# Optimization experiments

Measured on AMD Instinct MI355X. Metric: run time of the kernel, lower is better.

Reference implementation:

```python
import jax, jax.numpy as jnp
import numpy as np

WS = 7
NH = 4

def _rel_idx(ws):
    ch, cw = np.meshgrid(np.arange(ws), np.arange(ws), indexing='ij')
    cf = np.stack([ch.ravel(), cw.ravel()])  # [2, ws*ws]
    rel = cf[:, :, None] - cf[:, None, :]
    rel = rel.transpose(1, 2, 0)
    rel[:, :, 0] += ws - 1
    rel[:, :, 1] += ws - 1
    rel[:, :, 0] *= 2 * ws - 1
    return jnp.asarray(rel.sum(-1), dtype=jnp.int32)  # [N, N]

def layernorm(x, g, b, eps=1e-5):
    m = jnp.mean(x, -1, keepdims=True)
    v = jnp.var(x, -1, keepdims=True)
    return (x - m) * jax.lax.rsqrt(v + eps) * g + b

def setup_inputs() -> dict:
    key = jax.random.key(0)
    ks = jax.random.split(key, 8)
    B, HH, WW, C = 32, 56, 56, 128
    hid = 512
    s = 0.02
    return {
        'x': jax.random.normal(ks[0], (B, HH * WW, C), jnp.float32),
        'H': HH, 'W': WW,
        'norm1_g': jnp.ones((C,), jnp.float32),
        'norm1_b': jnp.zeros((C,), jnp.float32),
        'qkv_w': jax.random.normal(ks[1], (3 * C, C), jnp.float32) * s,
        'qkv_b': jnp.zeros((3 * C,), jnp.float32),
        'rel_bias_table': jax.random.normal(ks[2], ((2 * WS - 1) ** 2, NH), jnp.float32) * s,
        'rel_idx': _rel_idx(WS),
        'proj_w': jax.random.normal(ks[3], (C, C), jnp.float32) * s,
        'proj_b': jnp.zeros((C,), jnp.float32),
        'norm2_g': jnp.ones((C,), jnp.float32),
        'norm2_b': jnp.zeros((C,), jnp.float32),
        'mlp_w1': jax.random.normal(ks[4], (hid, C), jnp.float32) * s,
        'mlp_b1': jnp.zeros((hid,), jnp.float32),
        'mlp_w2': jax.random.normal(ks[5], (C, hid), jnp.float32) * s,
        'mlp_b2': jnp.zeros((C,), jnp.float32),
    }

def swin_block(x, H, W, norm1_g, norm1_b, qkv_w, qkv_b, rel_bias_table, rel_idx,
               proj_w, proj_b, norm2_g, norm2_b, mlp_w1, mlp_b1, mlp_w2, mlp_b2,
               shift=3, ws=WS, nh=NH):
    B, L, C = x.shape
    N = ws * ws
    hd = C // nh
    scale = hd ** -0.5
    shortcut = x
    h = layernorm(x, norm1_g, norm1_b).reshape(B, H, W, C)
    if shift > 0:
        h = jnp.roll(h, (-shift, -shift), axis=(1, 2))
    # window partition -> [B*nW, N, C]
    h = h.reshape(B, H // ws, ws, W // ws, ws, C).transpose(0, 1, 3, 2, 4, 5).reshape(-1, N, C)
    # attention (no mask in source forward)
    qkv = h @ qkv_w.T + qkv_b  # [B_, N, 3C]
    qkv = qkv.reshape(-1, N, 3, nh, hd).transpose(2, 0, 3, 1, 4)
    q, k, v = qkv[0] * scale, qkv[1], qkv[2]  # [B_, nh, N, hd]
    attn = jnp.einsum('bhnd,bhmd->bhnm', q, k)
    bias = rel_bias_table[rel_idx.reshape(-1)].reshape(N, N, nh).transpose(2, 0, 1)
    attn = jax.nn.softmax(attn + bias[None], axis=-1)
    o = jnp.einsum('bhnm,bhmd->bhnd', attn, v).transpose(0, 2, 1, 3).reshape(-1, N, C)
    o = o @ proj_w.T + proj_b
    # window reverse -> [B, H, W, C]
    o = o.reshape(B, H // ws, W // ws, ws, ws, C).transpose(0, 1, 3, 2, 4, 5).reshape(B, H, W, C)
    if shift > 0:
        o = jnp.roll(o, (shift, shift), axis=(1, 2))
    x = shortcut + o.reshape(B, L, C)
    h2 = layernorm(x, norm2_g, norm2_b)
    h2 = jax.nn.gelu(h2 @ mlp_w1.T + mlp_b1, approximate=False) @ mlp_w2.T + mlp_b2
    return x + h2

def reference(x, H, W, norm1_g, norm1_b, qkv_w, qkv_b, rel_bias_table, rel_idx,
              proj_w, proj_b, norm2_g, norm2_b, mlp_w1, mlp_b1, mlp_w2, mlp_b2):
    return swin_block(x, H, W, norm1_g, norm1_b, qkv_w, qkv_b, rel_bias_table, rel_idx,
                      proj_w, proj_b, norm2_g, norm2_b, mlp_w1, mlp_b1, mlp_w2, mlp_b2)
```

## Files before the change

kernel.cpp:

```cpp
#include <hip/hip_runtime.h>
#include <hip/hip_bf16.h>


#define NWIN 2048

typedef short short8  __attribute__((ext_vector_type(8)));
typedef short short4v __attribute__((ext_vector_type(4)));
typedef float f32x4   __attribute__((ext_vector_type(4)));

union Frag { int i[4]; unsigned u[4]; short8 s; };

#define QKVW_OFF  0
#define PROJW_OFF 49152
#define W1_OFF    65536
#define W2_OFF    131072
#define BIAS_BYTE_OFF 393216

__device__ __forceinline__ short f2bs(float v) {
  __hip_bfloat16 h = __float2bfloat16(v);
  union { __hip_bfloat16 h; short s; } u; u.h = h; return u.s;
}
__device__ __forceinline__ float gelu_f(float v) {
  float u = v * (0.7978845608028654f + 0.03567740814f * v * v);
  return v * __builtin_amdgcn_rcpf(1.f + __expf(-2.f * u));
}

__global__ __launch_bounds__(256) void conv_kernel(
    const float* __restrict__ qkvw, const float* __restrict__ projw,
    const float* __restrict__ w1,   const float* __restrict__ w2,
    const float* __restrict__ tab,  const int* __restrict__ ridx,
    __hip_bfloat16* __restrict__ wsb, float* __restrict__ biasT)
{
  int idx = blockIdx.x * 256 + threadIdx.x;
  if (idx < 49152)       wsb[QKVW_OFF + idx]          = __float2bfloat16(qkvw[idx]);
  else if (idx < 65536)  wsb[PROJW_OFF + idx - 49152] = __float2bfloat16(projw[idx - 49152]);
  else if (idx < 131072) wsb[W1_OFF + idx - 65536]    = __float2bfloat16(w1[idx - 65536]);
  else if (idx < 196608) wsb[W2_OFF + idx - 131072]   = __float2bfloat16(w2[idx - 131072]);
  else if (idx < 212992) {
    int i = idx - 196608;
    int h = i >> 12, m = (i >> 6) & 63, n = i & 63;
    biasT[i] = (m < 49 && n < 49) ? tab[ridx[n*49 + m]*4 + h] : 0.f;
  }
}

__global__ __launch_bounds__(512, 4) void fused_kernel(
    const float* __restrict__ x,
    const float* __restrict__ n1g, const float* __restrict__ n1b,
    const __hip_bfloat16* __restrict__ qkvwb, const float* __restrict__ qkvb,
    const float* __restrict__ biasT,
    const __hip_bfloat16* __restrict__ projwb, const float* __restrict__ projb,
    const float* __restrict__ n2g, const float* __restrict__ n2b,
    const __hip_bfloat16* __restrict__ w1b, const float* __restrict__ b1,
    const __hip_bfloat16* __restrict__ w2b, const float* __restrict__ b2,
    float* __restrict__ out)
{
  __shared__ alignas(16) __hip_bfloat16 hbuf[64][136];
  __shared__ alignas(16) char shmem[34816];
  __hip_bfloat16* const Kl  = (__hip_bfloat16*)shmem;
  __hip_bfloat16* const vTl = (__hip_bfloat16*)(shmem + 17408);
  float*          const x2s = (float*)shmem;
  __hip_bfloat16* const hbA = (__hip_bfloat16*)shmem;
  __hip_bfloat16* const hbB = (__hip_bfloat16*)(shmem + 17408);

  const int tid = threadIdx.x, wave = tid >> 6, lane = tid & 63;
  const int l15 = lane & 15, quad = lane >> 4;
  const int h = wave >> 1, half = wave & 1;
  const int b = blockIdx.x >> 6, wi = (blockIdx.x >> 3) & 7, wj = blockIdx.x & 7;

  {
    float g0 = n1g[lane], g1 = n1g[lane+64], e0 = n1b[lane], e1 = n1b[lane+64];
    float va[7], vb[7];
    #pragma unroll
    for (int i = 0; i < 7; ++i) {
      int n = wave + i*8;
      va[i] = 0.f; vb[i] = 0.f;
      if (n < 49) {
        int r = n / 7, c = n - r * 7;
        int si = wi*7 + r + 3; if (si >= 56) si -= 56;
        int sj = wj*7 + c + 3; if (sj >= 56) sj -= 56;
        const float* xr = x + (b*3136 + si*56 + sj) * 128;
        va[i] = xr[lane]; vb[i] = xr[lane + 64];
      }
    }
    #pragma unroll
    for (int i = 0; i < 7; ++i) {
      int n = wave + i*8;
      if (n < 49) {
        float s = va[i] + vb[i], sq = va[i]*va[i] + vb[i]*vb[i];
        #pragma unroll
        for (int off = 32; off > 0; off >>= 1) {
          s  += __shfl_xor(s,  off);
          sq += __shfl_xor(sq, off);
        }
        float mean = s * 0.0078125f;
        float var  = sq * 0.0078125f - mean*mean;
        float rstd = rsqrtf(var + 1e-5f);
        hbuf[n][lane]    = __float2bfloat16((va[i]-mean)*rstd*g0 + e0);
        hbuf[n][lane+64] = __float2bfloat16((vb[i]-mean)*rstd*g1 + e1);
      }
    }
  }
  __syncthreads();

  {
    f32x4 kacc[4] = {}, vacc[4] = {};
    #pragma unroll
    for (int ks = 0; ks < 4; ++ks) {
      short8 hf[4];
      #pragma unroll
      for (int mt = 0; mt < 4; ++mt)
        hf[mt] = *(const short8*)(&hbuf[mt*16 + l15][ks*32 + quad*8]);
      short8 wfk = *(const short8*)(qkvwb + (128 + wave*16 + l15)*128 + ks*32 + quad*8);
      short8 wfv = *(const short8*)(qkvwb + (256 + wave*16 + l15)*128 + ks*32 + quad*8);
      #pragma unroll
      for (int mt = 0; mt < 4; ++mt) {
        kacc[mt] = __builtin_amdgcn_mfma_f32_16x16x32_bf16(wfk, hf[mt], kacc[mt], 0, 0, 0);
        vacc[mt] = __builtin_amdgcn_mfma_f32_16x16x32_bf16(hf[mt], wfv, vacc[mt], 0, 0, 0);
      }
    }
    {
      const int fo = wave*16 + quad*4;
      float bb[4];
      #pragma unroll
      for (int r = 0; r < 4; ++r) bb[r] = qkvb[128 + fo + r];
      #pragma unroll
      for (int mt = 0; mt < 4; ++mt) {
        int m = mt*16 + l15;
        if (m < 49) {
          short4v pkv;
          #pragma unroll
          for (int r = 0; r < 4; ++r) pkv[r] = f2bs(kacc[mt][r] + bb[r]);
          *(short4v*)(Kl + m*136 + fo) = pkv;
        }
      }
    }
    {
      const int fv = wave*16 + l15;
      const int hh = wave >> 1, d = fv & 31;
      const float bia = qkvb[256 + fv];
      #pragma unroll
      for (int mt = 0; mt < 4; ++mt) {
        int m0 = mt*16 + quad*4;
        #pragma unroll
        for (int r = 0; r < 4; ++r) {
          int m = m0 + r;
          float v = (m < 49) ? (vacc[mt][r] + bia) : 0.f;
          vTl[(hh*32 + d)*64 + ((((m>>3) ^ (d & 7))) << 3) + (m & 7)] = __float2bfloat16(v);
        }
      }
    }
  }

  Frag qfr[2];
  {
    f32x4 qacc[2][2] = {};
    #pragma unroll
    for (int ks = 0; ks < 4; ++ks) {
      short8 hfq[2];
      #pragma unroll
      for (int nt = 0; nt < 2; ++nt)
        hfq[nt] = *(const short8*)(&hbuf[(half*2 + nt)*16 + l15][ks*32 + quad*8]);
      #pragma unroll
      for (int tq = 0; tq < 2; ++tq) {
        short8 wf = *(const short8*)(qkvwb + ((h*2 + tq)*16 + l15)*128 + ks*32 + quad*8);
        #pragma unroll
        for (int nt = 0; nt < 2; ++nt)
          qacc[tq][nt] = __builtin_amdgcn_mfma_f32_16x16x32_bf16(wf, hfq[nt], qacc[tq][nt], 0, 0, 0);
      }
    }
    const float qs = 0.17677669529663687f;
    unsigned pkq[2][2][2];
    #pragma unroll
    for (int tq = 0; tq < 2; ++tq) {
      float bb[4];
      #pragma unroll
      for (int r = 0; r < 4; ++r) bb[r] = qkvb[h*32 + tq*16 + quad*4 + r];
      #pragma unroll
      for (int nt = 0; nt < 2; ++nt)
        #pragma unroll
        for (int i = 0; i < 2; ++i) {
          unsigned lo = (unsigned short)f2bs((qacc[tq][nt][2*i]   + bb[2*i])   * qs);
          unsigned hi = (unsigned short)f2bs((qacc[tq][nt][2*i+1] + bb[2*i+1]) * qs);
          pkq[tq][nt][i] = lo | (hi << 16);
        }
    }
    #pragma unroll
    for (int nt = 0; nt < 2; ++nt)
      #pragma unroll
      for (int p = 0; p < 4; ++p) {
        int sl = (((quad & 1)*2 + (p >> 1)) << 4) | l15;
        int a  = __shfl((int)pkq[0][nt][p & 1], sl);
        int c2 = __shfl((int)pkq[1][nt][p & 1], sl);
        qfr[nt].i[p] = (quad >= 2) ? c2 : a;
      }
  }
  __syncthreads();

  {
    short8 kf[4];
    #pragma unroll
    for (int mt = 0; mt < 4; ++mt)
      kf[mt] = *(const short8*)(Kl + (mt*16 + l15)*136 + h*32 + quad*8);

    f32x4 sacc[4][2] = {};
    #pragma unroll
    for (int mt = 0; mt < 4; ++mt)
      #pragma unroll
      for (int nc = 0; nc < 2; ++nc)
        sacc[mt][nc] = __builtin_amdgcn_mfma_f32_16x16x32_bf16(kf[mt], qfr[nc].s, sacc[mt][nc], 0, 0, 0);

    const float* bT = biasT + h*4096;
    #pragma unroll
    for (int mt = 0; mt < 4; ++mt)
      #pragma unroll
      for (int nc = 0; nc < 2; ++nc)
        #pragma unroll
        for (int r = 0; r < 4; ++r)
          sacc[mt][nc][r] += bT[(mt*16 + quad*4 + r)*64 + (half*2 + nc)*16 + l15];

    unsigned pk[4][2][2];
    #pragma unroll
    for (int nc = 0; nc < 2; ++nc) {
      float mx = -1e30f;
      #pragma unroll
      for (int mt = 0; mt < 3; ++mt)
        #pragma unroll
        for (int r = 0; r < 4; ++r) mx = fmaxf(mx, sacc[mt][nc][r]);
      mx = fmaxf(mx, (quad == 0) ? sacc[3][nc][0] : -1e30f);
      mx = fmaxf(mx, __shfl_xor(mx, 16));
      mx = fmaxf(mx, __shfl_xor(mx, 32));
      float sum = 0.f;
      #pragma unroll
      for (int mt = 0; mt < 3; ++mt)
        #pragma unroll
        for (int r = 0; r < 4; ++r) {
          float e = __expf(sacc[mt][nc][r] - mx);
          sacc[mt][nc][r] = e; sum += e;
        }
      {
        float e = (quad == 0) ? __expf(sacc[3][nc][0] - mx) : 0.f;
        sacc[3][nc][0] = e; sacc[3][nc][1] = 0.f; sacc[3][nc][2] = 0.f; sacc[3][nc][3] = 0.f;
        sum += e;
      }
      sum += __shfl_xor(sum, 16);
      sum += __shfl_xor(sum, 32);
      float inv = 1.f / sum;
      #pragma unroll
      for (int mt = 0; mt < 4; ++mt)
        #pragma unroll
        for (int i = 0; i < 2; ++i) {
          unsigned lo = (unsigned short)f2bs(sacc[mt][nc][2*i]   * inv);
          unsigned hi = (unsigned short)f2bs(sacc[mt][nc][2*i+1] * inv);
          pk[mt][nc][i] = lo | (hi << 16);
        }
    }
    Frag pfr[2][2];
    #pragma unroll
    for (int kt = 0; kt < 2; ++kt)
      #pragma unroll
      for (int nc = 0; nc < 2; ++nc)
        #pragma unroll
        for (int p = 0; p < 4; ++p) {
          int sl = (((quad & 1)*2 + (p >> 1)) << 4) | l15;
          int a  = __shfl((int)pk[kt*2    ][nc][p & 1], sl);
          int c2 = __shfl((int)pk[kt*2 + 1][nc][p & 1], sl);
          pfr[kt][nc].i[p] = (quad >= 2) ? c2 : a;
        }

    f32x4 oacc[2][2] = {};
    #pragma unroll
    for (int kt = 0; kt < 2; ++kt) {
      short8 vf[2];
      #pragma unroll
      for (int dt = 0; dt < 2; ++dt)
        vf[dt] = *(const short8*)(vTl + (h*32 + dt*16 + l15)*64 + (((kt*4 + quad) ^ (l15 & 7)) << 3));
      #pragma unroll
      for (int dt = 0; dt < 2; ++dt)
        #pragma unroll
        for (int nc = 0; nc < 2; ++nc)
          oacc[dt][nc] = __builtin_amdgcn_mfma_f32_16x16x32_bf16(vf[dt], pfr[kt][nc].s, oacc[dt][nc], 0, 0, 0);
    }
    #pragma unroll
    for (int dt = 0; dt < 2; ++dt)
      #pragma unroll
      for (int nc = 0; nc < 2; ++nc) {
        int n = (half*2 + nc)*16 + l15;
        if (n < 49) {
          short4v pkv;
          #pragma unroll
          for (int r = 0; r < 4; ++r) pkv[r] = f2bs(oacc[dt][nc][r]);
          *(short4v*)(&hbuf[n][h*32 + dt*16 + quad*4]) = pkv;
        }
      }
  }
  __syncthreads();

  f32x4 x2v[4];
  {
    const int n = wave * 16 + l15;
    float xres[4][4];
    #pragma unroll
    for (int mt = 0; mt < 4; ++mt) {
      #pragma unroll
      for (int r = 0; r < 4; ++r) {
        int m = mt*16 + quad*4 + r;
        float v = 0.f;
        if (m < 49) {
          int rr = m / 7, cc = m - rr * 7;
          int si = wi*7 + rr + 3; if (si >= 56) si -= 56;
          int sj = wj*7 + cc + 3; if (sj >= 56) sj -= 56;
          v = x[(b*3136 + si*56 + sj) * 128 + n];
        }
        xres[mt][r] = v;
      }
    }
    f32x4 acc[4] = {};
    #pragma unroll
    for (int ks = 0; ks < 4; ++ks) {
      short8 af[4];
      #pragma unroll
      for (int mt = 0; mt < 4; ++mt)
        af[mt] = *(const short8*)(&hbuf[mt*16 + l15][ks*32 + quad*8]);
      short8 bfr = *(const short8*)(projwb + n*128 + ks*32 + quad*8);
      #pragma unroll
      for (int mt = 0; mt < 4; ++mt)
        acc[mt] = __builtin_amdgcn_mfma_f32_16x16x32_bf16(af[mt], bfr, acc[mt], 0, 0, 0);
    }
    float pbv = projb[n];
    #pragma unroll
    for (int mt = 0; mt < 4; ++mt) {
      #pragma unroll
      for (int r = 0; r < 4; ++r) {
        int m = mt*16 + quad*4 + r;
        float v = 0.f;
        if (m < 49) v = acc[mt][r] + pbv + xres[mt][r];
        x2v[mt][r] = v;
        x2s[m*132 + n] = v;
      }
    }
  }
  __syncthreads();

  {
    float g0 = n2g[lane], g1 = n2g[lane+64], e0 = n2b[lane], e1 = n2b[lane+64];
    for (int n = wave; n < 49; n += 8) {
      float v0 = x2s[n*132 + lane], v1 = x2s[n*132 + lane + 64];
      float s = v0 + v1, sq = v0*v0 + v1*v1;
      #pragma unroll
      for (int off = 32; off > 0; off >>= 1) {
        s  += __shfl_xor(s,  off);
        sq += __shfl_xor(sq, off);
      }
      float mean = s * 0.0078125f;
      float var  = sq * 0.0078125f - mean*mean;
      float rstd = rsqrtf(var + 1e-5f);
      hbuf[n][lane]    = __float2bfloat16((v0-mean)*rstd*g0 + e0);
      hbuf[n][lane+64] = __float2bfloat16((v1-mean)*rstd*g1 + e1);
    }
    __hip_bfloat16 z = __float2bfloat16(0.f);
    for (int n = 49 + wave; n < 64; n += 8) {
      hbuf[n][lane] = z; hbuf[n][lane+64] = z;
    }
  }
  __syncthreads();

  f32x4 acc2[4] = {};
  const int fb2 = wave * 16;

  auto G1 = [&](int c, __hip_bfloat16* dst) {
    const int jg = c*128 + wave*16;
    f32x4 a1[4] = {};
    #pragma unroll
    for (int ks = 0; ks < 4; ++ks) {
      short8 lf[4];
      #pragma unroll
      for (int mt = 0; mt < 4; ++mt)
        lf[mt] = *(const short8*)(&hbuf[mt*16 + l15][ks*32 + quad*8]);
      short8 wf = *(const short8*)(w1b + (jg + l15)*128 + ks*32 + quad*8);
      #pragma unroll
      for (int mt = 0; mt < 4; ++mt)
        a1[mt] = __builtin_amdgcn_mfma_f32_16x16x32_bf16(wf, lf[mt], a1[mt], 0, 0, 0);
    }
    float bb[4];
    #pragma unroll
    for (int r = 0; r < 4; ++r) bb[r] = b1[jg + quad*4 + r];
    #pragma unroll
    for (int mt = 0; mt < 4; ++mt) {
      int m = mt*16 + l15;
      short4v pkv;
      #pragma unroll
      for (int r = 0; r < 4; ++r) pkv[r] = f2bs(gelu_f(a1[mt][r] + bb[r]));
      *(short4v*)(dst + m*136 + wave*16 + quad*4) = pkv;
    }
  };
  auto G2 = [&](int c, const __hip_bfloat16* src) {
    #pragma unroll
    for (int ks = 0; ks < 4; ++ks) {
      short8 af[4];
      #pragma unroll
      for (int mt = 0; mt < 4; ++mt)
        af[mt] = *(const short8*)(src + (mt*16 + l15)*136 + ks*32 + quad*8);
      short8 wf = *(const short8*)(w2b + (fb2 + l15)*512 + c*128 + ks*32 + quad*8);
      #pragma unroll
      for (int mt = 0; mt < 4; ++mt)
        acc2[mt] = __builtin_amdgcn_mfma_f32_16x16x32_bf16(af[mt], wf, acc2[mt], 0, 0, 0);
    }
  };

  G1(0, hbA);
  __syncthreads();
  G1(1, hbB); G2(0, hbA);
  __syncthreads();
  G1(2, hbA); G2(1, hbB);
  __syncthreads();
  G1(3, hbB); G2(2, hbA);
  __syncthreads();
  G2(3, hbB);

  {
    const int f = fb2 + l15;
    const float bb = b2[f];
    #pragma unroll
    for (int mt = 0; mt < 4; ++mt) {
      #pragma unroll
      for (int r = 0; r < 4; ++r) {
        int m = mt*16 + quad*4 + r;
        if (m < 49) {
          int rr = m / 7, cc = m - rr * 7;
          int si = wi*7 + rr + 3; if (si >= 56) si -= 56;
          int sj = wj*7 + cc + 3; if (sj >= 56) sj -= 56;
          int o = (b*3136 + si*56 + sj) * 128 + f;
          out[o] = acc2[mt][r] + bb + x2v[mt][r];
        }
      }
    }
  }
}

extern "C" void kernel_launch(void* const* d_in, const int* in_sizes, int n_in,
                              void* d_out, int out_size, void* d_ws, size_t ws_size,
                              hipStream_t stream) {
  const float* x     = (const float*)d_in[0];
  const float* n1g   = (const float*)d_in[3];
  const float* n1b   = (const float*)d_in[4];
  const float* qkvw  = (const float*)d_in[5];
  const float* qkvb  = (const float*)d_in[6];
  const float* tab   = (const float*)d_in[7];
  const int*   ridx  = (const int*)d_in[8];
  const float* projw = (const float*)d_in[9];
  const float* projb = (const float*)d_in[10];
  const float* n2g   = (const float*)d_in[11];
  const float* n2b   = (const float*)d_in[12];
  const float* w1    = (const float*)d_in[13];
  const float* b1    = (const float*)d_in[14];
  const float* w2    = (const float*)d_in[15];
  const float* b2    = (const float*)d_in[16];
  float* outp = (float*)d_out;

  __hip_bfloat16* wsb = (__hip_bfloat16*)d_ws;
  float* biasT = (float*)((char*)d_ws + BIAS_BYTE_OFF);

  hipLaunchKernelGGL(conv_kernel, dim3(832), dim3(256), 0, stream,
                     qkvw, projw, w1, w2, tab, ridx, wsb, biasT);
  hipLaunchKernelGGL(fused_kernel, dim3(NWIN), dim3(512), 0, stream,
                     x, n1g, n1b, wsb + QKVW_OFF, qkvb, biasT, wsb + PROJW_OFF, projb,
                     n2g, n2b, wsb + W1_OFF, b1, wsb + W2_OFF, b2, outp);
}
```

Before: 256.3 us.

## Compute per-head K/V in registers, drop LDS staging and a barrier

Each wave now computes the K and V projections for its own head directly into MFMA fragment registers via lane shuffles, instead of computing a slice of K/V and staging it through LDS. This removes the LDS K/V buffers and one block barrier. The attention output goes to a separate LDS buffer and the residual is stored as bf16. LayerNorm-2 statistics are reduced from per-wave partial sums in a small shared table. The cost is redundant K/V computation: two waves per head each compute the full K/V, doubling that MFMA work. Occupancy hint is lowered from 4 to 2 blocks, and LN2 now normalizes bf16-rounded residual values, which slightly changes numerics.

```diff
diff --git a/kernel.cpp b/kernel.cpp
--- a/kernel.cpp
+++ b/kernel.cpp
@@ -20,6 +20,7 @@
   __hip_bfloat16 h = __float2bfloat16(v);
   union { __hip_bfloat16 h; short s; } u; u.h = h; return u.s;
 }
+__device__ __forceinline__ float bs2f(__hip_bfloat16 h) { return __bfloat162float(h); }
 __device__ __forceinline__ float gelu_f(float v) {
   float u = v * (0.7978845608028654f + 0.03567740814f * v * v);
   return v * __builtin_amdgcn_rcpf(1.f + __expf(-2.f * u));
@@ -43,7 +44,7 @@
   }
 }
 
-__global__ __launch_bounds__(512, 4) void fused_kernel(
+__global__ __launch_bounds__(512, 2) void fused_kernel(
     const float* __restrict__ x,
     const float* __restrict__ n1g, const float* __restrict__ n1b,
     const __hip_bfloat16* __restrict__ qkvwb, const float* __restrict__ qkvb,
@@ -56,9 +57,9 @@
 {
   __shared__ alignas(16) __hip_bfloat16 hbuf[64][136];
   __shared__ alignas(16) char shmem[34816];
-  __hip_bfloat16* const Kl  = (__hip_bfloat16*)shmem;
-  __hip_bfloat16* const vTl = (__hip_bfloat16*)(shmem + 17408);
-  float*          const x2s = (float*)shmem;
+  __shared__ float pt[64][9][2];
+  __hip_bfloat16* const oB  = (__hip_bfloat16*)shmem;
+  __hip_bfloat16* const x2b = (__hip_bfloat16*)(shmem + 17408);
   __hip_bfloat16* const hbA = (__hip_bfloat16*)shmem;
   __hip_bfloat16* const hbB = (__hip_bfloat16*)(shmem + 17408);
 
@@ -102,56 +103,8 @@
   }
   __syncthreads();
 
-  {
-    f32x4 kacc[4] = {}, vacc[4] = {};
-    #pragma unroll
-    for (int ks = 0; ks < 4; ++ks) {
-      short8 hf[4];
-      #pragma unroll
-      for (int mt = 0; mt < 4; ++mt)
-        hf[mt] = *(const short8*)(&hbuf[mt*16 + l15][ks*32 + quad*8]);
-      short8 wfk = *(const short8*)(qkvwb + (128 + wave*16 + l15)*128 + ks*32 + quad*8);
-      short8 wfv = *(const short8*)(qkvwb + (256 + wave*16 + l15)*128 + ks*32 + quad*8);
-      #pragma unroll
-      for (int mt = 0; mt < 4; ++mt) {
-        kacc[mt] = __builtin_amdgcn_mfma_f32_16x16x32_bf16(wfk, hf[mt], kacc[mt], 0, 0, 0);
-        vacc[mt] = __builtin_amdgcn_mfma_f32_16x16x32_bf16(hf[mt], wfv, vacc[mt], 0, 0, 0);
-      }
-    }
-    {
-      const int fo = wave*16 + quad*4;
-      float bb[4];
-      #pragma unroll
-      for (int r = 0; r < 4; ++r) bb[r] = qkvb[128 + fo + r];
-      #pragma unroll
-      for (int mt = 0; mt < 4; ++mt) {
-        int m = mt*16 + l15;
-        if (m < 49) {
-          short4v pkv;
-          #pragma unroll
-          for (int r = 0; r < 4; ++r) pkv[r] = f2bs(kacc[mt][r] + bb[r]);
-          *(short4v*)(Kl + m*136 + fo) = pkv;
-        }
-      }
-    }
-    {
-      const int fv = wave*16 + l15;
-      const int hh = wave >> 1, d = fv & 31;
-      const float bia = qkvb[256 + fv];
-      #pragma unroll
-      for (int mt = 0; mt < 4; ++mt) {
-        int m0 = mt*16 + quad*4;
-        #pragma unroll
-        for (int r = 0; r < 4; ++r) {
-          int m = m0 + r;
-          float v = (m < 49) ? (vacc[mt][r] + bia) : 0.f;
-          vTl[(hh*32 + d)*64 + ((((m>>3) ^ (d & 7))) << 3) + (m & 7)] = __float2bfloat16(v);
-        }
-      }
-    }
-  }
-
-  Frag qfr[2];
+  Frag qfr[2], kfr[4], vfr[2][2];
+
   {
     f32x4 qacc[2][2] = {};
     #pragma unroll
@@ -162,7 +115,7 @@
         hfq[nt] = *(const short8*)(&hbuf[(half*2 + nt)*16 + l15][ks*32 + quad*8]);
       #pragma unroll
       for (int tq = 0; tq < 2; ++tq) {
-        short8 wf = *(const short8*)(qkvwb + ((h*2 + tq)*16 + l15)*128 + ks*32 + quad*8);
+        short8 wf = *(const short8*)(qkvwb + (h*32 + tq*16 + l15)*128 + ks*32 + quad*8);
         #pragma unroll
         for (int nt = 0; nt < 2; ++nt)
           qacc[tq][nt] = __builtin_amdgcn_mfma_f32_16x16x32_bf16(wf, hfq[nt], qacc[tq][nt], 0, 0, 0);
@@ -194,20 +147,101 @@
         qfr[nt].i[p] = (quad >= 2) ? c2 : a;
       }
   }
-  __syncthreads();
-
-  {
-    short8 kf[4];
+
+  {
+    f32x4 kacc[2][4] = {};
+    #pragma unroll
+    for (int ks = 0; ks < 4; ++ks) {
+      short8 hf[4];
+      #pragma unroll
+      for (int mt = 0; mt < 4; ++mt)
+        hf[mt] = *(const short8*)(&hbuf[mt*16 + l15][ks*32 + quad*8]);
+      #pragma unroll
+      for (int tq = 0; tq < 2; ++tq) {
+        short8 wf = *(const short8*)(qkvwb + (128 + h*32 + tq*16 + l15)*128 + ks*32 + quad*8);
+        #pragma unroll
+        for (int mt = 0; mt < 4; ++mt)
+          kacc[tq][mt] = __builtin_amdgcn_mfma_f32_16x16x32_bf16(wf, hf[mt], kacc[tq][mt], 0, 0, 0);
+      }
+    }
+    unsigned pkk[2][4][2];
+    #pragma unroll
+    for (int tq = 0; tq < 2; ++tq) {
+      float bb[4];
+      #pragma unroll
+      for (int r = 0; r < 4; ++r) bb[r] = qkvb[128 + h*32 + tq*16 + quad*4 + r];
+      #pragma unroll
+      for (int mt = 0; mt < 4; ++mt)
+        #pragma unroll
+        for (int i = 0; i < 2; ++i) {
+          unsigned lo = (unsigned short)f2bs(kacc[tq][mt][2*i]   + bb[2*i]);
+          unsigned hi = (unsigned short)f2bs(kacc[tq][mt][2*i+1] + bb[2*i+1]);
+          pkk[tq][mt][i] = lo | (hi << 16);
+        }
+    }
     #pragma unroll
     for (int mt = 0; mt < 4; ++mt)
-      kf[mt] = *(const short8*)(Kl + (mt*16 + l15)*136 + h*32 + quad*8);
-
+      #pragma unroll
+      for (int p = 0; p < 4; ++p) {
+        int sl = (((quad & 1)*2 + (p >> 1)) << 4) | l15;
+        int a  = __shfl((int)pkk[0][mt][p & 1], sl);
+        int c2 = __shfl((int)pkk[1][mt][p & 1], sl);
+        kfr[mt].i[p] = (quad >= 2) ? c2 : a;
+      }
+  }
+
+  {
+    f32x4 vacc[4][2] = {};
+    #pragma unroll
+    for (int ks = 0; ks < 4; ++ks) {
+      short8 hf[4];
+      #pragma unroll
+      for (int mt = 0; mt < 4; ++mt)
+        hf[mt] = *(const short8*)(&hbuf[mt*16 + l15][ks*32 + quad*8]);
+      #pragma unroll
+      for (int dt = 0; dt < 2; ++dt) {
+        short8 wf = *(const short8*)(qkvwb + (256 + h*32 + dt*16 + l15)*128 + ks*32 + quad*8);
+        #pragma unroll
+        for (int mt = 0; mt < 4; ++mt)
+          vacc[mt][dt] = __builtin_amdgcn_mfma_f32_16x16x32_bf16(hf[mt], wf, vacc[mt][dt], 0, 0, 0);
+      }
+    }
+    unsigned pkvv[4][2][2];
+    #pragma unroll
+    for (int dt = 0; dt < 2; ++dt) {
+      float bia = qkvb[256 + h*32 + dt*16 + l15];
+      #pragma unroll
+      for (int mt = 0; mt < 4; ++mt)
+        #pragma unroll
+        for (int i = 0; i < 2; ++i) {
+          int m0 = mt*16 + quad*4;
+          float v0 = (m0 + 2*i     < 49) ? (vacc[mt][dt][2*i]   + bia) : 0.f;
+          float v1 = (m0 + 2*i + 1 < 49) ? (vacc[mt][dt][2*i+1] + bia) : 0.f;
+          unsigned lo = (unsigned short)f2bs(v0);
+          unsigned hi = (unsigned short)f2bs(v1);
+          pkvv[mt][dt][i] = lo | (hi << 16);
+        }
+    }
+    #pragma unroll
+    for (int kt = 0; kt < 2; ++kt)
+      #pragma unroll
+      for (int dt = 0; dt < 2; ++dt)
+        #pragma unroll
+        for (int p = 0; p < 4; ++p) {
+          int sl = (((quad & 1)*2 + (p >> 1)) << 4) | l15;
+          int a  = __shfl((int)pkvv[kt*2    ][dt][p & 1], sl);
+          int c2 = __shfl((int)pkvv[kt*2 + 1][dt][p & 1], sl);
+          vfr[kt][dt].i[p] = (quad >= 2) ? c2 : a;
+        }
+  }
+
+  {
     f32x4 sacc[4][2] = {};
     #pragma unroll
     for (int mt = 0; mt < 4; ++mt)
       #pragma unroll
       for (int nc = 0; nc < 2; ++nc)
-        sacc[mt][nc] = __builtin_amdgcn_mfma_f32_16x16x32_bf16(kf[mt], qfr[nc].s, sacc[mt][nc], 0, 0, 0);
+        sacc[mt][nc] = __builtin_amdgcn_mfma_f32_16x16x32_bf16(kfr[mt].s, qfr[nc].s, sacc[mt][nc], 0, 0, 0);
 
     const float* bT = biasT + h*4096;
     #pragma unroll
@@ -269,17 +303,12 @@
 
     f32x4 oacc[2][2] = {};
     #pragma unroll
-    for (int kt = 0; kt < 2; ++kt) {
-      short8 vf[2];
+    for (int kt = 0; kt < 2; ++kt)
       #pragma unroll
       for (int dt = 0; dt < 2; ++dt)
-        vf[dt] = *(const short8*)(vTl + (h*32 + dt*16 + l15)*64 + (((kt*4 + quad) ^ (l15 & 7)) << 3));
-      #pragma unroll
-      for (int dt = 0; dt < 2; ++dt)
         #pragma unroll
         for (int nc = 0; nc < 2; ++nc)
-          oacc[dt][nc] = __builtin_amdgcn_mfma_f32_16x16x32_bf16(vf[dt], pfr[kt][nc].s, oacc[dt][nc], 0, 0, 0);
-    }
+          oacc[dt][nc] = __builtin_amdgcn_mfma_f32_16x16x32_bf16(vfr[kt][dt].s, pfr[kt][nc].s, oacc[dt][nc], 0, 0, 0);
     #pragma unroll
     for (int dt = 0; dt < 2; ++dt)
       #pragma unroll
@@ -289,7 +318,7 @@
           short4v pkv;
           #pragma unroll
           for (int r = 0; r < 4; ++r) pkv[r] = f2bs(oacc[dt][nc][r]);
-          *(short4v*)(&hbuf[n][h*32 + dt*16 + quad*4]) = pkv;
+          *(short4v*)(oB + n*136 + h*32 + dt*16 + quad*4) = pkv;
         }
       }
   }
@@ -320,7 +349,7 @@
       short8 af[4];
       #pragma unroll
       for (int mt = 0; mt < 4; ++mt)
-        af[mt] = *(const short8*)(&hbuf[mt*16 + l15][ks*32 + quad*8]);
+        af[mt] = *(const short8*)(oB + (mt*16 + l15)*136 + ks*32 + quad*8);
       short8 bfr = *(const short8*)(projwb + n*128 + ks*32 + quad*8);
       #pragma unroll
       for (int mt = 0; mt < 4; ++mt)
@@ -335,7 +364,23 @@
         float v = 0.f;
         if (m < 49) v = acc[mt][r] + pbv + xres[mt][r];
         x2v[mt][r] = v;
-        x2s[m*132 + n] = v;
+        x2b[m*136 + n] = __float2bfloat16(v);
+      }
+    }
+    #pragma unroll
+    for (int mt = 0; mt < 4; ++mt) {
+      #pragma unroll
+      for (int r = 0; r < 4; ++r) {
+        float s = x2v[mt][r], q = s * s;
+        #pragma unroll
+        for (int off = 1; off < 16; off <<= 1) {
+          s += __shfl_xor(s, off);
+          q += __shfl_xor(q, off);
+        }
+        if (l15 == 0) {
+          int m = mt*16 + quad*4 + r;
+          pt[m][wave][0] = s; pt[m][wave][1] = q;
+        }
       }
     }
   }
@@ -344,16 +389,13 @@
   {
     float g0 = n2g[lane], g1 = n2g[lane+64], e0 = n2b[lane], e1 = n2b[lane+64];
     for (int n = wave; n < 49; n += 8) {
-      float v0 = x2s[n*132 + lane], v1 = x2s[n*132 + lane + 64];
-      float s = v0 + v1, sq = v0*v0 + v1*v1;
-      #pragma unroll
-      for (int off = 32; off > 0; off >>= 1) {
-        s  += __shfl_xor(s,  off);
-        sq += __shfl_xor(sq, off);
-      }
+      float s = 0.f, q = 0.f;
+      #pragma unroll
+      for (int w = 0; w < 8; ++w) { s += pt[n][w][0]; q += pt[n][w][1]; }
       float mean = s * 0.0078125f;
-      float var  = sq * 0.0078125f - mean*mean;
+      float var  = q * 0.0078125f - mean*mean;
       float rstd = rsqrtf(var + 1e-5f);
+      float v0 = bs2f(x2b[n*136 + lane]), v1 = bs2f(x2b[n*136 + lane + 64]);
       hbuf[n][lane]    = __float2bfloat16((v0-mean)*rstd*g0 + e0);
       hbuf[n][lane+64] = __float2bfloat16((v1-mean)*rstd*g1 + e1);
     }
```

New measurement: 329.6 us. +28.6%, slower.
